# Kernel optimization log

Measured on AMD Instinct MI355X. Metric: run time of the kernel, lower is better.

## Reference

```python
import jax, jax.numpy as jnp
import numpy as np

BINS = 10
MMT = 0.9
N = 33554432  # 2^25 elements


def setup_inputs() -> dict:
    key = jax.random.key(0)
    k1, k2, k3 = jax.random.split(key, 3)
    pred = jax.random.normal(k1, (N,), dtype=jnp.float32)
    target = jax.random.randint(k2, (N,), 0, 2, dtype=jnp.int32)
    acc_sum = jax.random.uniform(k3, (BINS,), dtype=jnp.float32)
    return {"pred": pred, "target": target, "acc_sum": acc_sum}


def reference(pred, target, acc_sum):
    bins = acc_sum.shape[0]
    # border = arange(bins+1)/bins, with last edge nudged up by 1e-6
    border = jnp.arange(bins + 1, dtype=jnp.float32) / bins
    border = border.at[-1].add(1e-6)

    t = target.astype(jnp.float32)
    # gradient density measure on detached predictions
    g = jnp.abs(jax.nn.sigmoid(jax.lax.stop_gradient(pred)) - t)
    # bin index: g in [border[i], border[i+1])  ->  i
    idx = jnp.clip(jnp.searchsorted(border, g, side='right') - 1, 0, bins - 1)

    # single-pass histogram (replaces the per-bin mask loop)
    counts = jax.ops.segment_sum(jnp.ones_like(g), idx, num_segments=bins)
    nonempty = counts > 0

    # momentum-accumulated bin statistics (only updated for non-empty bins)
    acc_new = jnp.where(nonempty, MMT * acc_sum + (1.0 - MMT) * counts, acc_sum)

    tot = jnp.float32(max(pred.shape[0], 1.0))
    safe_acc = jnp.where(nonempty, acc_new, 1.0)
    bin_w = jnp.where(nonempty, tot / safe_acc, 0.0)  # [bins]

    n = jnp.sum(nonempty.astype(jnp.float32))
    bin_w = jnp.where(n > 0, bin_w / jnp.maximum(n, 1.0), bin_w)

    # per-element GHM weights are constants w.r.t. pred (buffer + detached g)
    w = jax.lax.stop_gradient(bin_w[idx])

    # BCE-with-logits, numerically stable
    bce = jnp.maximum(pred, 0.0) - pred * t + jnp.log1p(jnp.exp(-jnp.abs(pred)))
    return jnp.sum(w * bce) / tot
```

## Files before the change

### kernel.cpp

```cpp
#include <hip/hip_runtime.h>

#define BINS 10
#define NTHREADS 256


__device__ __forceinline__ float wave_reduce_add(float v) {
#pragma unroll
    for (int off = 32; off > 0; off >>= 1) v += __shfl_down(v, off, 64);
    return v;
}

__global__ __launch_bounds__(NTHREADS) void ghm_pass1(
    const float* __restrict__ pred, const int* __restrict__ target,
    float* __restrict__ g_sum,
    unsigned int* __restrict__ g_cnt,
    int n4, int n)
{
    __shared__ float s_cnt[BINS][NTHREADS];
    __shared__ float s_sum[BINS][NTHREADS];

    const int tid = threadIdx.x;
#pragma unroll
    for (int b = 0; b < BINS; ++b) { s_cnt[b][tid] = 0.f; s_sum[b][tid] = 0.f; }
    __syncthreads();

    const float4* __restrict__ p4 = reinterpret_cast<const float4*>(pred);
    const int4*   __restrict__ t4 = reinterpret_cast<const int4*>(target);

    const int gtid   = blockIdx.x * blockDim.x + tid;
    const int stride = gridDim.x * blockDim.x;

    for (int i = gtid; i < n4; i += stride) {
        const float4 xv = p4[i];
        const int4   tv = t4[i];
        const float xs[4] = {xv.x, xv.y, xv.z, xv.w};
        const int   ts[4] = {tv.x, tv.y, tv.z, tv.w};
#pragma unroll
        for (int j = 0; j < 4; ++j) {
            const float x    = xs[j];
            const bool  tpos = (ts[j] != 0);
            const float E   = __expf(-fabsf(x));
            const float r   = 1.0f + E;
            const float inv = __builtin_amdgcn_rcpf(r);
            const bool  cond = ((x >= 0.0f) == tpos);
            const float g    = cond ? (E * inv) : inv;
            const float bce = fmaxf(x, 0.0f) - (tpos ? x : 0.0f) + __logf(r);
            int k = (int)(g * 10.0f);
            k = (k > BINS - 1) ? (BINS - 1) : k;

            s_cnt[k][tid] += 1.0f;
            s_sum[k][tid] += bce;
        }
    }

    if (gtid == 0) {
        for (int i = n4 * 4; i < n; ++i) {
            const float x    = pred[i];
            const bool  tpos = (target[i] != 0);
            const float E   = __expf(-fabsf(x));
            const float r   = 1.0f + E;
            const float inv = __builtin_amdgcn_rcpf(r);
            const bool  cond = ((x >= 0.0f) == tpos);
            const float g    = cond ? (E * inv) : inv;
            const float bce = fmaxf(x, 0.0f) - (tpos ? x : 0.0f) + __logf(r);
            int k = (int)(g * 10.0f);
            k = (k > BINS - 1) ? (BINS - 1) : k;
            s_cnt[k][tid] += 1.0f;
            s_sum[k][tid] += bce;
        }
    }
    __syncthreads();

    __shared__ float r_sum[BINS];
    __shared__ float r_cnt[BINS];
    if (tid < BINS) { r_sum[tid] = 0.f; r_cnt[tid] = 0.f; }
    __syncthreads();

    const int lane = tid & 63;
#pragma unroll
    for (int b = 0; b < BINS; ++b) {
        const float v = wave_reduce_add(s_sum[b][tid]);
        const float c = wave_reduce_add(s_cnt[b][tid]);
        if (lane == 0) { atomicAdd(&r_sum[b], v); atomicAdd(&r_cnt[b], c); }
    }
    __syncthreads();

    if (tid < BINS) {
        atomicAdd(&g_sum[tid], r_sum[tid]);
        atomicAdd(&g_cnt[tid], (unsigned int)(r_cnt[tid] + 0.5f));
    }
}

__global__ void ghm_finalize(const float* __restrict__ g_sum,
                             const unsigned int* __restrict__ g_cnt,
                             const float* __restrict__ acc_sum,
                             float* __restrict__ out, float tot)
{
    if (threadIdx.x == 0 && blockIdx.x == 0) {
        float binw[BINS];
        int n = 0;
#pragma unroll
        for (int b = 0; b < BINS; ++b) {
            const float c  = (float)g_cnt[b];
            const bool  ne = (c > 0.0f);
            const float accn = ne ? (0.9f * acc_sum[b] + 0.1f * c) : acc_sum[b];
            binw[b] = ne ? (tot / accn) : 0.0f;
            n += ne ? 1 : 0;
        }
        const float scale = (n > 0) ? (1.0f / (float)n) : 1.0f;
        float res = 0.0f;
#pragma unroll
        for (int b = 0; b < BINS; ++b) res += (binw[b] * scale) * g_sum[b];
        out[0] = res / tot;
    }
}

extern "C" void kernel_launch(void* const* d_in, const int* in_sizes, int n_in,
                              void* d_out, int out_size, void* d_ws, size_t ws_size,
                              hipStream_t stream) {
    const float* pred    = (const float*)d_in[0];
    const int*   target  = (const int*)d_in[1];
    const float* acc_sum = (const float*)d_in[2];
    float*       out     = (float*)d_out;

    const int n  = in_sizes[0];
    const int n4 = n / 4;

    float*        g_sum = (float*)d_ws;
    unsigned int* g_cnt = (unsigned int*)((float*)d_ws + BINS);

    hipMemsetAsync(d_ws, 0, 2 * BINS * sizeof(float), stream);

    ghm_pass1<<<2048, NTHREADS, 0, stream>>>(pred, target, g_sum, g_cnt, n4, n);

    const float tot = (float)(n > 1 ? n : 1);
    ghm_finalize<<<1, 64, 0, stream>>>(g_sum, g_cnt, acc_sum, out, tot);
}
```

Baseline: 99.71 us.

## Simplify GHM math via sign flip and share LDS histogram columns with atomics

Rewrites the per-element computation using a sign-flipped logit y, so that g = 1 - sigmoid(y) and bce = -log(sigmoid(y)). This removes the abs, the select logic and one add per element. The shared histogram is halved to 128 columns, with two threads sharing each column through LDS atomic adds. That cuts LDS footprint (better occupancy) and the final reduce work, but adds atomic contention and makes float accumulation order nondeterministic. The -log(q) form may lose precision for large |x|.

```diff
diff --git a/kernel.cpp b/kernel.cpp
--- a/kernel.cpp
+++ b/kernel.cpp
@@ -2,6 +2,7 @@
 
 #define BINS 10
 #define NTHREADS 256
+#define COLS 128
 
 
 __device__ __forceinline__ float wave_reduce_add(float v) {
@@ -16,12 +17,19 @@
     unsigned int* __restrict__ g_cnt,
     int n4, int n)
 {
-    __shared__ float s_cnt[BINS][NTHREADS];
-    __shared__ float s_sum[BINS][NTHREADS];
+    __shared__ float s_cnt[BINS][COLS];
+    __shared__ float s_sum[BINS][COLS];
+    __shared__ float r_sum[BINS];
+    __shared__ float r_cnt[BINS];
 
     const int tid = threadIdx.x;
-#pragma unroll
-    for (int b = 0; b < BINS; ++b) { s_cnt[b][tid] = 0.f; s_sum[b][tid] = 0.f; }
+    const int col = tid & (COLS - 1);
+
+    for (int i = tid; i < BINS * COLS; i += NTHREADS) {
+        (&s_cnt[0][0])[i] = 0.f;
+        (&s_sum[0][0])[i] = 0.f;
+    }
+    if (tid < BINS) { r_sum[tid] = 0.f; r_cnt[tid] = 0.f; }
     __syncthreads();
 
     const float4* __restrict__ p4 = reinterpret_cast<const float4*>(pred);
@@ -37,51 +45,45 @@
         const int   ts[4] = {tv.x, tv.y, tv.z, tv.w};
 #pragma unroll
         for (int j = 0; j < 4; ++j) {
-            const float x    = xs[j];
-            const bool  tpos = (ts[j] != 0);
-            const float E   = __expf(-fabsf(x));
-            const float r   = 1.0f + E;
-            const float inv = __builtin_amdgcn_rcpf(r);
-            const bool  cond = ((x >= 0.0f) == tpos);
-            const float g    = cond ? (E * inv) : inv;
-            const float bce = fmaxf(x, 0.0f) - (tpos ? x : 0.0f) + __logf(r);
+            const float x = xs[j];
+            const int   t = ts[j];
+            const float y = __int_as_float(__float_as_int(x) ^ ((t ^ 1) << 31));
+            const float E   = __expf(-y);
+            const float q   = __builtin_amdgcn_rcpf(1.0f + E);
+            const float g   = 1.0f - q;
+            const float bce = -__logf(q);
             int k = (int)(g * 10.0f);
             k = (k > BINS - 1) ? (BINS - 1) : k;
-
-            s_cnt[k][tid] += 1.0f;
-            s_sum[k][tid] += bce;
+            atomicAdd(&s_cnt[k][col], 1.0f);
+            atomicAdd(&s_sum[k][col], bce);
         }
     }
 
     if (gtid == 0) {
         for (int i = n4 * 4; i < n; ++i) {
-            const float x    = pred[i];
-            const bool  tpos = (target[i] != 0);
-            const float E   = __expf(-fabsf(x));
-            const float r   = 1.0f + E;
-            const float inv = __builtin_amdgcn_rcpf(r);
-            const bool  cond = ((x >= 0.0f) == tpos);
-            const float g    = cond ? (E * inv) : inv;
-            const float bce = fmaxf(x, 0.0f) - (tpos ? x : 0.0f) + __logf(r);
+            const float x = pred[i];
+            const int   t = target[i];
+            const float y = __int_as_float(__float_as_int(x) ^ ((t ^ 1) << 31));
+            const float E   = __expf(-y);
+            const float q   = __builtin_amdgcn_rcpf(1.0f + E);
+            const float g   = 1.0f - q;
+            const float bce = -__logf(q);
             int k = (int)(g * 10.0f);
             k = (k > BINS - 1) ? (BINS - 1) : k;
-            s_cnt[k][tid] += 1.0f;
-            s_sum[k][tid] += bce;
+            atomicAdd(&s_cnt[k][col], 1.0f);
+            atomicAdd(&s_sum[k][col], bce);
         }
     }
     __syncthreads();
 
-    __shared__ float r_sum[BINS];
-    __shared__ float r_cnt[BINS];
-    if (tid < BINS) { r_sum[tid] = 0.f; r_cnt[tid] = 0.f; }
-    __syncthreads();
-
-    const int lane = tid & 63;
+    if (tid < COLS) {
+        const int lane = tid & 63;
 #pragma unroll
-    for (int b = 0; b < BINS; ++b) {
-        const float v = wave_reduce_add(s_sum[b][tid]);
-        const float c = wave_reduce_add(s_cnt[b][tid]);
-        if (lane == 0) { atomicAdd(&r_sum[b], v); atomicAdd(&r_cnt[b], c); }
+        for (int b = 0; b < BINS; ++b) {
+            const float v = wave_reduce_add(s_sum[b][tid]);
+            const float c = wave_reduce_add(s_cnt[b][tid]);
+            if (lane == 0) { atomicAdd(&r_sum[b], v); atomicAdd(&r_cnt[b], c); }
+        }
     }
     __syncthreads();
 
```

Measured after the change: 366.5 us. 3.68x slower.
